# Kernel tuning notes

Measured on AMD Instinct MI355X. Metric: run time of the kernel, lower is better.

The kernel has to match this reference:

```python
import jax, jax.numpy as jnp
import numpy as np

B, T_ENC, FEAT, H, W2V, T_DEC, V = 32, 80, 4096, 256, 256, 30, 32000


def lstm_cell(x, h, c, w_ih, w_hh, b_ih, b_hh):
    # PyTorch LSTMCell: gates order i, f, g, o
    g = x @ w_ih.T + h @ w_hh.T + b_ih + b_hh
    i, f, gg, o = jnp.split(g, 4, axis=-1)
    c_new = jax.nn.sigmoid(f) * c + jax.nn.sigmoid(i) * jnp.tanh(gg)
    h_new = jax.nn.sigmoid(o) * jnp.tanh(c_new)
    return h_new, c_new


def setup_inputs() -> dict:
    key = jax.random.key(0)
    ks = jax.random.split(key, 13)
    s = 0.05
    return {
        'feat': jax.random.normal(ks[0], (B, T_ENC, FEAT), jnp.float32),
        'caption': jax.random.normal(ks[1], (B, T_DEC, W2V), jnp.float32),
        'caption_one_hot': jax.random.normal(ks[2], (B, T_DEC, V), jnp.float32),
        'keep_rate': 1,
        'w_ih1': jax.random.normal(ks[3], (4 * H, FEAT), jnp.float32) * s,
        'w_hh1': jax.random.normal(ks[4], (4 * H, H), jnp.float32) * s,
        'b_ih1': jax.random.normal(ks[5], (4 * H,), jnp.float32) * s,
        'b_hh1': jax.random.normal(ks[6], (4 * H,), jnp.float32) * s,
        'w_ih2': jax.random.normal(ks[7], (4 * H, H + W2V), jnp.float32) * s,
        'w_hh2': jax.random.normal(ks[8], (4 * H, H), jnp.float32) * s,
        'b_ih2': jax.random.normal(ks[9], (4 * H,), jnp.float32) * s,
        'b_hh2': jax.random.normal(ks[10], (4 * H,), jnp.float32) * s,
        'w_out': jax.random.normal(ks[11], (V, H), jnp.float32) * s,
        'b_out': jax.random.normal(ks[12], (V,), jnp.float32) * s,
    }


def reference(feat, caption, caption_one_hot, keep_rate,
              w_ih1, w_hh1, b_ih1, b_hh1,
              w_ih2, w_hh2, b_ih2, b_hh2,
              w_out, b_out):
    zeros_h = jnp.zeros((B, H), feat.dtype)
    pad1 = jnp.zeros((B, FEAT), feat.dtype)

    # ---------------- encoder: 80 steps ----------------
    def enc_step(carry, x_t):
        h1, c1, h2, c2 = carry
        h1, c1 = lstm_cell(x_t, h1, c1, w_ih1, w_hh1, b_ih1, b_hh1)
        h2, c2 = lstm_cell(jnp.concatenate([zeros_h, h1], axis=1), h2, c2,
                           w_ih2, w_hh2, b_ih2, b_hh2)
        return (h1, c1, h2, c2), h2

    (h1, c1, h2, c2), enc_h2 = jax.lax.scan(
        enc_step, (zeros_h, zeros_h, zeros_h, zeros_h),
        jnp.transpose(feat, (1, 0, 2)))
    enc_h2 = jnp.transpose(enc_h2, (1, 0, 2))  # [B, 80, H]

    # ---------------- decoder: teacher forcing (coin>=100 never fires) ----
    targets = jnp.argmax(caption_one_hot, axis=-1)  # [B, T_DEC]

    def dec_step(carry, xs):
        h1, c1, h2, c2, loss = carry
        word_t, tgt_t = xs  # [B, W2V], [B]
        h1, c1 = lstm_cell(pad1, h1, c1, w_ih1, w_hh1, b_ih1, b_hh1)
        h2n, c2 = lstm_cell(jnp.concatenate([word_t, h1], axis=1), h2, c2,
                            w_ih2, w_hh2, b_ih2, b_hh2)
        logits = h2n @ w_out.T + b_out  # [B, V]
        logp = jax.nn.log_softmax(logits, axis=-1)
        ce = -jnp.take_along_axis(logp, tgt_t[:, None], axis=1)[:, 0]
        loss = loss + jnp.mean(ce) / B  # sum(mean-CE)/batch, per original
        # attention: scores of encoder h2 states against current h2
        attn = jax.nn.softmax(jnp.einsum('bsh,bh->bs', enc_h2, h2n), axis=-1)
        ctx = jnp.einsum('bs,bsh->bh', attn, enc_h2)  # replaces h2 for next step
        return (h1, c1, ctx, c2, loss), None

    xs = (jnp.transpose(caption[:, :T_DEC - 1, :], (1, 0, 2)),
          jnp.transpose(targets[:, 1:T_DEC], (1, 0)))
    (h1, c1, h2, c2, total_loss), _ = jax.lax.scan(
        dec_step, (h1, c1, h2, c2, jnp.float32(0.0)), xs)
    return total_loss
```

## Files before the change

### kernel.cpp

```cpp
#include <hip/hip_runtime.h>
#include <hip/hip_bf16.h>
#include <math.h>

#define BB 32
#define TE 80
#define FEAT 4096
#define HH 256
#define W2V 256
#define TD 30
#define VV 32000
#define G4 1024

typedef unsigned short u16;
typedef unsigned int u32;
using f32x4 = __attribute__((ext_vector_type(4))) float;
using bf16x8 = __attribute__((ext_vector_type(8))) short;
using f16x2 = __attribute__((ext_vector_type(2))) _Float16;

#define SENT 0xFFFFFFFFu
#define NANF 0x7FC00000u

__device__ __forceinline__ float sigm(float x) { return 1.0f / (1.0f + expf(-x)); }
__device__ __forceinline__ u16 f2bf(float f) {
  u32 u = __float_as_uint(f);
  u32 r = (u + 0x7FFFu + ((u >> 16) & 1u)) >> 16;
  return (u16)r;
}
__device__ __forceinline__ u32 packh2(float lo, float hi) {
  f16x2 v = {(_Float16)lo, (_Float16)hi};
  return __builtin_bit_cast(u32, v);
}

#define AT_LOAD(p)     __hip_atomic_load((p), __ATOMIC_RELAXED, __HIP_MEMORY_SCOPE_AGENT)
#define AT_STORE(p, v) __hip_atomic_store((p), (v), __ATOMIC_RELAXED, __HIP_MEMORY_SCOPE_AGENT)

__device__ __forceinline__ float fdot2h(f16x2 a, f16x2 b, float c) {
#if __has_builtin(__builtin_amdgcn_fdot2)
  return __builtin_amdgcn_fdot2(a, b, c, false);
#else
  return c + (float)a[0] * (float)b[0] + (float)a[1] * (float)b[1];
#endif
}

__global__ __launch_bounds__(256) void prep_kernel(
    const float* __restrict__ feat, const float* __restrict__ w_ih1,
    const float* __restrict__ w_ih2, const float* __restrict__ caption,
    const float* __restrict__ onehot,
    const float* __restrict__ b_ih1, const float* __restrict__ b_hh1,
    const float* __restrict__ b_ih2, const float* __restrict__ b_hh2,
    u16* __restrict__ featb, u16* __restrict__ w_ih1b,
    u16* __restrict__ w_ih2lb, u16* __restrict__ capb,
    float* __restrict__ bias1, float* __restrict__ bias2,
    u32* __restrict__ H1H, u32* __restrict__ H2H, u32* __restrict__ A2P,
    float* __restrict__ loss, int* __restrict__ ctrs,
    int* __restrict__ targets) {
  int blk = blockIdx.x, tid = threadIdx.x;
  if (blk < 928) {
    int k = blk;
    int s = (k >> 5) + 1, b = k & 31;
    const float* row = &onehot[((size_t)b * TD + s) * VV];
    float bv = -INFINITY;
    int bi = 0x7fffffff;
    for (int v = tid; v < VV; v += 256) {
      float x = row[v];
      if (x > bv || (x == bv && v < bi)) { bv = x; bi = v; }
    }
    __shared__ float sv[256];
    __shared__ int si[256];
    sv[tid] = bv; si[tid] = bi;
    __syncthreads();
    for (int off = 128; off; off >>= 1) {
      if (tid < off) {
        float ov = sv[tid + off]; int oi = si[tid + off];
        if (ov > sv[tid] || (ov == sv[tid] && oi < si[tid])) { sv[tid] = ov; si[tid] = oi; }
      }
      __syncthreads();
    }
    if (tid == 0) targets[k] = si[0];
  } else if (blk < 3488) {
    int i0 = (blk - 928) * 1024 + tid;
#pragma unroll
    for (int ii = 0; ii < 4; ++ii) {
      int i = i0 + ii * 256;
      float4 v = *(const float4*)&feat[(size_t)i * 4];
      *(ushort4*)&featb[(size_t)i * 4] =
          make_ushort4(f2bf(v.x), f2bf(v.y), f2bf(v.z), f2bf(v.w));
    }
  } else if (blk < 4512) {
    int i0 = (blk - 3488) * 1024 + tid;
#pragma unroll
    for (int ii = 0; ii < 4; ++ii) {
      int i = i0 + ii * 256;
      float4 v = *(const float4*)&w_ih1[(size_t)i * 4];
      *(ushort4*)&w_ih1b[(size_t)i * 4] =
          make_ushort4(f2bf(v.x), f2bf(v.y), f2bf(v.z), f2bf(v.w));
    }
  } else if (blk < 4576) {
    int i0 = (blk - 4512) * 1024 + tid;
#pragma unroll
    for (int ii = 0; ii < 4; ++ii) {
      int i = i0 + ii * 256;
      int row = i >> 6, c = (i & 63) * 4;
      float4 v = *(const float4*)&w_ih2[(size_t)row * 512 + c];
      *(ushort4*)&w_ih2lb[(size_t)row * 256 + c] =
          make_ushort4(f2bf(v.x), f2bf(v.y), f2bf(v.z), f2bf(v.w));
    }
  } else if (blk < 4636) {
    int i0 = (blk - 4576) * 1024 + tid;
#pragma unroll
    for (int ii = 0; ii < 4; ++ii) {
      int i = i0 + ii * 256;
      float4 v = *(const float4*)&caption[(size_t)i * 4];
      *(ushort4*)&capb[(size_t)i * 4] =
          make_ushort4(f2bf(v.x), f2bf(v.y), f2bf(v.z), f2bf(v.w));
    }
  } else if (blk < 5076) {
    int i = (blk - 4636) * 256 + tid;
    uint4 z = {0u, 0u, 0u, 0u};
    uint4 s = {SENT, SENT, SENT, SENT};
    uint4 v = (i < 1024) ? z : s;
    ((uint4*)H1H)[i] = v;
    ((uint4*)H2H)[i] = v;
  } else if (blk < 5956) {
    int i0 = (blk - 5076) * 1024 + tid;
    uint4 s = {NANF, NANF, NANF, NANF};
#pragma unroll
    for (int ii = 0; ii < 4; ++ii) ((uint4*)A2P)[i0 + ii * 256] = s;
  } else {
    for (int i = tid; i < 1024; i += 256) {
      bias1[i] = b_ih1[i] + b_hh1[i];
      bias2[i] = b_ih2[i] + b_hh2[i];
    }
    if (tid == 0) { *loss = 0.0f; ctrs[0] = 0; ctrs[32] = 0; }
  }
}

#define GBM 128
#define GBN 128
#define GBK 64
#define LDSTR 72

__device__ void gemm_x1_body(char* smem, int bx, int by,
                             const u16* __restrict__ Ab, const u16* __restrict__ Bw,
                             const float* __restrict__ bias, float* __restrict__ C) {
  u16* As = (u16*)smem;
  u16* Bs = (u16*)(smem + 18432);
  int tid = threadIdx.x;
  int rBase = by * GBM;
  int nBase = bx * GBN;
  int lane = tid & 63, w = tid >> 6;
  int wrow = (w >> 1) * 64, wcol = (w & 1) * 64;
  int lrow = lane & 15, lk = (lane >> 4) * 8;

  f32x4 acc[4][4];
#pragma unroll
  for (int m = 0; m < 4; ++m)
#pragma unroll
    for (int n = 0; n < 4; ++n) acc[m][n] = (f32x4){0.f, 0.f, 0.f, 0.f};

  for (int k0 = 0; k0 < FEAT; k0 += GBK) {
#pragma unroll
    for (int i = 0; i < 4; ++i) {
      int f = i * 256 + tid;
      int r = f >> 3, c8 = f & 7;
      *(uint4*)&As[r * LDSTR + c8 * 8] =
          *(const uint4*)&Ab[(size_t)(rBase + r) * FEAT + k0 + c8 * 8];
    }
#pragma unroll
    for (int i = 0; i < 4; ++i) {
      int f = i * 256 + tid;
      int r = f >> 3, c8 = f & 7;
      *(uint4*)&Bs[r * LDSTR + c8 * 8] =
          *(const uint4*)&Bw[(size_t)(nBase + r) * FEAT + k0 + c8 * 8];
    }
    __syncthreads();
#pragma unroll
    for (int s2 = 0; s2 < 2; ++s2) {
      bf16x8 af[4], bfr[4];
#pragma unroll
      for (int m = 0; m < 4; ++m)
        af[m] = *(const bf16x8*)&As[(wrow + m * 16 + lrow) * LDSTR + s2 * 32 + lk];
#pragma unroll
      for (int n = 0; n < 4; ++n)
        bfr[n] = *(const bf16x8*)&Bs[(wcol + n * 16 + lrow) * LDSTR + s2 * 32 + lk];
#pragma unroll
      for (int m = 0; m < 4; ++m)
#pragma unroll
        for (int n = 0; n < 4; ++n)
          acc[m][n] = __builtin_amdgcn_mfma_f32_16x16x32_bf16(
              af[m], bfr[n], acc[m][n], 0, 0, 0);
    }
    __syncthreads();
  }
  int orow = (lane >> 4) * 4;
  int ocol = lane & 15;
#pragma unroll
  for (int m = 0; m < 4; ++m)
#pragma unroll
    for (int n = 0; n < 4; ++n) {
      int cidx = nBase + wcol + n * 16 + ocol;
      float bv = bias[cidx];
#pragma unroll
      for (int q = 0; q < 4; ++q) {
        int r = rBase + wrow + m * 16 + orow + q;
        C[(size_t)r * G4 + cidx] = acc[m][n][q] + bv;
      }
    }
}

__device__ void xw2_body(char* smem, int nb, int t,
                         const u16* __restrict__ capb, const u16* __restrict__ w_ih2lb,
                         const float* __restrict__ bias2, float* __restrict__ XW2) {
  u16* As = (u16*)smem;
  u16* Bs = (u16*)(smem + 16896);
  int tid = threadIdx.x;
  int nBase = nb * 64;
#pragma unroll
  for (int it = 0; it < 4; ++it) {
    int i = it * 256 + tid;
    int r = i >> 5, c8 = i & 31;
    *(uint4*)&As[r * 264 + c8 * 8] =
        *(const uint4*)&capb[((size_t)r * TD + t) * 256 + c8 * 8];
  }
#pragma unroll
  for (int it = 0; it < 8; ++it) {
    int i = it * 256 + tid;
    int r = i >> 5, c8 = i & 31;
    *(uint4*)&Bs[r * 264 + c8 * 8] =
        *(const uint4*)&w_ih2lb[(size_t)(nBase + r) * 256 + c8 * 8];
  }
  __syncthreads();
  int lane = tid & 63, w = tid >> 6;
  int lrow = lane & 15, lk = (lane >> 4) * 8;
  f32x4 acc[2];
  acc[0] = (f32x4){0.f, 0.f, 0.f, 0.f};
  acc[1] = (f32x4){0.f, 0.f, 0.f, 0.f};
#pragma unroll
  for (int ks = 0; ks < 8; ++ks) {
    bf16x8 bfr = *(const bf16x8*)&Bs[(w * 16 + lrow) * 264 + ks * 32 + lk];
#pragma unroll
    for (int m = 0; m < 2; ++m) {
      bf16x8 af = *(const bf16x8*)&As[(m * 16 + lrow) * 264 + ks * 32 + lk];
      acc[m] = __builtin_amdgcn_mfma_f32_16x16x32_bf16(af, bfr, acc[m], 0, 0, 0);
    }
  }
  int col = nBase + w * 16 + (lane & 15);
  float bv = bias2[col];
  int orow = (lane >> 4) * 4;
#pragma unroll
  for (int m = 0; m < 2; ++m)
#pragma unroll
    for (int q = 0; q < 4; ++q) {
      int bb = m * 16 + orow + q;
      XW2[((size_t)t * 32 + bb) * G4 + col] = acc[m][q] + bv;
    }
}

__global__ __launch_bounds__(256) void gemms_kernel(
    const u16* __restrict__ featb, const u16* __restrict__ w_ih1b,
    const float* __restrict__ bias1, float* __restrict__ X1,
    const u16* __restrict__ capb, const u16* __restrict__ w_ih2lb,
    const float* __restrict__ bias2, float* __restrict__ XW2) {
  __shared__ __align__(16) char smem[50688];
  int blk = blockIdx.x;
  if (blk < 160) {
    gemm_x1_body(smem, blk & 7, blk >> 3, featb, w_ih1b, bias1, X1);
  } else {
    int k = blk - 160;
    xw2_body(smem, k & 15, k >> 4, capb, w_ih2lb, bias2, XW2);
  }
}

struct RP {
  const float *X1, *XW2, *bias1, *bias2;
  const float *w_hh1, *w_ih2, *w_hh2;
  u32* H1H;
  u32* H2H;
  u32* A2P;
  u16* H2NB;
};

__global__ __launch_bounds__(512, 1) void recurrent_kernel(RP p) {
  __shared__ float encL[TE][257];
  __shared__ __align__(16) f16x2 hS[128];
  __shared__ float tmp2[256];
  __shared__ float gb[256];
  __shared__ float a2pS[256];
  __shared__ float hnew[64];
  __shared__ float sc[80];
  __shared__ float red[4];
  int bid = blockIdx.x, tid = threadIdx.x;
  bool isL1 = bid < 128;
  int lb = isL1 ? bid : bid - 128;
  int b = lb >> 2, q = lb & 3;
  int r2 = tid >> 1, half = tid & 1;
  int g = r2 >> 6, jj = r2 & 63;
  int grow = (g << 8) + (q << 6) + jj;
  int jf = (q << 6) + tid;

  if (isL1) {
    f16x2 wA[64], wB[64];
    {
      const float4* sA = (const float4*)(p.w_hh1 + (size_t)grow * 256 + half * 128);
      const float4* sB = (const float4*)(p.w_ih2 + (size_t)grow * 512 + 256 + half * 128);
#pragma unroll
      for (int k = 0; k < 32; ++k) {
        float4 v = sA[k];
        wA[k * 2 + 0] = f16x2{(_Float16)v.x, (_Float16)v.y};
        wA[k * 2 + 1] = f16x2{(_Float16)v.z, (_Float16)v.w};
        float4 u = sB[k];
        wB[k * 2 + 0] = f16x2{(_Float16)u.x, (_Float16)u.y};
        wB[k * 2 + 1] = f16x2{(_Float16)u.z, (_Float16)u.w};
      }
    }
    float c1 = 0.f;
    float b1v0 = 0, b1v1 = 0, b1v2 = 0, b1v3 = 0;
    if (tid < 64) {
      b1v0 = p.bias1[jf]; b1v1 = p.bias1[256 + jf];
      b1v2 = p.bias1[512 + jf]; b1v3 = p.bias1[768 + jf];
    }
    for (int T = 0; T <= 109; ++T) {
      float x0 = b1v0, x1 = b1v1, x2 = b1v2, x3 = b1v3;
      if (tid < 64 && T < TE) {
        const float* xb = &p.X1[((size_t)b * TE + T) * G4 + jf];
        x0 = xb[0]; x1 = xb[256]; x2 = xb[512]; x3 = xb[768];
      }
      if (tid < 128) {
        const u32* src = &p.H1H[((size_t)T * 32 + b) * 128 + tid];
        u32 v = AT_LOAD(src);
        int gd = 0;
        while (v == SENT && ++gd < (1 << 24)) {
          __builtin_amdgcn_s_sleep(1);
          v = AT_LOAD(src);
        }
        hS[tid] = __builtin_bit_cast(f16x2, v);
      }
      __syncthreads();
      float a1 = 0.f, a2 = 0.f;
      {
        const uint4* hv = ((const uint4*)hS) + half * 16;
#pragma unroll
        for (int k = 0; k < 16; ++k) {
          uint4 uu = hv[k];
          f16x2 e0 = __builtin_bit_cast(f16x2, uu.x), e1 = __builtin_bit_cast(f16x2, uu.y);
          f16x2 e2 = __builtin_bit_cast(f16x2, uu.z), e3 = __builtin_bit_cast(f16x2, uu.w);
          a1 = fdot2h(e0, wA[k * 4 + 0], a1);
          a2 = fdot2h(e0, wB[k * 4 + 0], a2);
          a1 = fdot2h(e1, wA[k * 4 + 1], a1);
          a2 = fdot2h(e1, wB[k * 4 + 1], a2);
          a1 = fdot2h(e2, wA[k * 4 + 2], a1);
          a2 = fdot2h(e2, wB[k * 4 + 2], a2);
          a1 = fdot2h(e3, wA[k * 4 + 3], a1);
          a2 = fdot2h(e3, wB[k * 4 + 3], a2);
        }
      }
      a1 += __shfl_xor(a1, 1);
      a2 += __shfl_xor(a2, 1);
      if (half == 0) {
        gb[r2] = a1;
        if (T >= 1)
          AT_STORE(&p.A2P[((size_t)T * 32 + b) * 1024 + grow], __float_as_uint(a2));
      }
      __syncthreads();
      if (T <= 108) {
        if (tid < 64) {
          float gi = gb[tid] + x0;
          float gf = gb[64 + tid] + x1;
          float gG = gb[128 + tid] + x2;
          float go = gb[192 + tid] + x3;
          c1 = sigm(gf) * c1 + sigm(gi) * tanhf(gG);
          hnew[tid] = sigm(go) * tanhf(c1);
        }
        if (tid < 32) {
          u32 pk = packh2(hnew[2 * tid], hnew[2 * tid + 1]);
          AT_STORE(&p.H1H[((size_t)(T + 1) * 32 + b) * 128 + (q << 5) + tid], pk);
        }
      }
    }
  } else {
    f16x2 wC[64];
    {
      const float4* sC = (const float4*)(p.w_hh2 + (size_t)grow * 256 + half * 128);
#pragma unroll
      for (int k = 0; k < 32; ++k) {
        float4 u = sC[k];
        wC[k * 2 + 0] = f16x2{(_Float16)u.x, (_Float16)u.y};
        wC[k * 2 + 1] = f16x2{(_Float16)u.z, (_Float16)u.w};
      }
    }
    float c2 = 0.f;
    float b2v0 = 0, b2v1 = 0, b2v2 = 0, b2v3 = 0;
    if (tid < 64) {
      b2v0 = p.bias2[jf]; b2v1 = p.bias2[256 + jf];
      b2v2 = p.bias2[512 + jf]; b2v3 = p.bias2[768 + jf];
    }
    for (int U = 1; U <= 109; ++U) {
      float x0 = b2v0, x1 = b2v1, x2 = b2v2, x3 = b2v3;
      if (tid < 64 && U >= 81) {
        const float* xb = &p.XW2[((size_t)(U - 81) * 32 + b) * G4 + jf];
        x0 = xb[0]; x1 = xb[256]; x2 = xb[512]; x3 = xb[768];
      }
      if (tid < 128) {
        const u32* src = &p.H2H[((size_t)(U - 1) * 32 + b) * 128 + tid];
        u32 v = AT_LOAD(src);
        int gd = 0;
        while (v == SENT && ++gd < (1 << 26)) v = AT_LOAD(src);
        f16x2 hp = __builtin_bit_cast(f16x2, v);
        hS[tid] = hp;
        tmp2[2 * tid] = (float)hp[0];
        tmp2[2 * tid + 1] = (float)hp[1];
      } else if (tid < 384) {
        int rr = tid - 128;
        int growp = ((rr >> 6) << 8) + (q << 6) + (rr & 63);
        const u32* src = &p.A2P[((size_t)U * 32 + b) * 1024 + growp];
        u32 v = AT_LOAD(src);
        int gd = 0;
        while (v == NANF && ++gd < (1 << 24)) {
          __builtin_amdgcn_s_sleep(1);
          v = AT_LOAD(src);
        }
        a2pS[rr] = __uint_as_float(v);
      }
      __syncthreads();
      float a2p0 = 0, a2p1 = 0, a2p2 = 0, a2p3 = 0;
      if (tid < 64) {
        a2p0 = a2pS[tid]; a2p1 = a2pS[64 + tid];
        a2p2 = a2pS[128 + tid]; a2p3 = a2pS[192 + tid];
      }
      if (U <= 81) {
        if (U >= 2 && tid < 256) encL[U - 2][tid] = tmp2[tid];
      } else {
        float a = 0.f;
        if (tid < TE) {
          const float* e = &encL[tid][0];
#pragma unroll 8
          for (int k2 = 0; k2 < 256; ++k2) a += e[k2] * tmp2[k2];
        }
        float av = (tid < TE) ? a : -INFINITY;
#pragma unroll
        for (int d = 32; d; d >>= 1) av = fmaxf(av, __shfl_xor(av, d));
        if (tid == 0) red[0] = av;
        if (tid == 64) red[1] = av;
        __syncthreads();
        float m = fmaxf(red[0], red[1]);
        float e2 = (tid < TE) ? expf(a - m) : 0.f;
        float sv = e2;
#pragma unroll
        for (int d = 32; d; d >>= 1) sv += __shfl_xor(sv, d);
        if (tid == 0) red[2] = sv;
        if (tid == 64) red[3] = sv;
        __syncthreads();
        float inv = 1.0f / (red[2] + red[3]);
        if (tid < TE) sc[tid] = e2 * inv;
        __syncthreads();
        if (tid < 256) {
          float acc = 0.f;
          for (int t2 = 0; t2 < TE; ++t2) acc += sc[t2] * encL[t2][tid];
          tmp2[tid] = acc;
        }
        __syncthreads();
        if (tid < 128)
          hS[tid] = f16x2{(_Float16)tmp2[2 * tid], (_Float16)tmp2[2 * tid + 1]};
        __syncthreads();
      }
      float a2 = 0.f;
      {
        const uint4* hv = ((const uint4*)hS) + half * 16;
#pragma unroll
        for (int k = 0; k < 16; ++k) {
          uint4 uu = hv[k];
          a2 = fdot2h(__builtin_bit_cast(f16x2, uu.x), wC[k * 4 + 0], a2);
          a2 = fdot2h(__builtin_bit_cast(f16x2, uu.y), wC[k * 4 + 1], a2);
          a2 = fdot2h(__builtin_bit_cast(f16x2, uu.z), wC[k * 4 + 2], a2);
          a2 = fdot2h(__builtin_bit_cast(f16x2, uu.w), wC[k * 4 + 3], a2);
        }
      }
      a2 += __shfl_xor(a2, 1);
      if (half == 0) gb[r2] = a2;
      __syncthreads();
      if (tid < 64) {
        float gi = gb[tid] + a2p0 + x0;
        float gf = gb[64 + tid] + a2p1 + x1;
        float gG = gb[128 + tid] + a2p2 + x2;
        float go = gb[192 + tid] + a2p3 + x3;
        c2 = sigm(gf) * c2 + sigm(gi) * tanhf(gG);
        float h = sigm(go) * tanhf(c2);
        hnew[tid] = h;
        if (U >= 81)
          p.H2NB[((size_t)(U - 81) * 32 + b) * 256 + jf] = f2bf(h);
      }
      if (tid < 32) {
        u32 pk = packh2(hnew[2 * tid], hnew[2 * tid + 1]);
        AT_STORE(&p.H2H[((size_t)U * 32 + b) * 128 + (q << 5) + tid], pk);
      }
    }
  }
}

__global__ __launch_bounds__(256, 1) void logits_final_kernel(
    const u16* __restrict__ H2NB, const float* __restrict__ w_out,
    const float* __restrict__ b_out, const int* __restrict__ targets,
    u32* __restrict__ pmaxA, u32* __restrict__ psumA, u32* __restrict__ tgtv,
    float* __restrict__ loss, int* __restrict__ ctrs, float* __restrict__ out) {
  __shared__ __align__(16) u16 bS[32768];
  __shared__ __align__(16) u16 aS[32 * 264];
  __shared__ int tS[32];
  __shared__ float sm[256];
  int tid = threadIdx.x, bid = blockIdx.x;
#pragma unroll
  for (int it = 0; it < 16; ++it) {
    int id = it * 256 + tid;
    int nt = id >> 9, rr = (id >> 5) & 15, kg = id & 31;
    int n = bid * 128 + nt * 16 + rr;
    const float* src = &w_out[(size_t)n * 256 + kg * 8];
    float4 v0 = *(const float4*)src;
    float4 v1 = *(const float4*)(src + 4);
    u16* dst = &bS[(size_t)((nt * 32 + kg) * 16 + rr) * 8];
    *(ushort4*)dst = make_ushort4(f2bf(v0.x), f2bf(v0.y), f2bf(v0.z), f2bf(v0.w));
    *(ushort4*)(dst + 4) = make_ushort4(f2bf(v1.x), f2bf(v1.y), f2bf(v1.z), f2bf(v1.w));
  }
  int wid = tid >> 6, lane = tid & 63, lcol = lane & 15, lk = lane >> 4;
  float bo[2];
#pragma unroll
  for (int n = 0; n < 2; ++n) bo[n] = b_out[(bid * 8 + wid * 2 + n) * 16 + lcol];

  for (int rg = 0; rg < 29; ++rg) {
    __syncthreads();
    for (int i = tid; i < 1024; i += 256) {
      int r = i >> 5, c8 = i & 31;
      *(uint4*)&aS[r * 264 + c8 * 8] =
          *(const uint4*)&H2NB[(size_t)rg * 8192 + r * 256 + c8 * 8];
    }
    if (tid < 32) tS[tid] = targets[rg * 32 + tid];
    __syncthreads();
    f32x4 acc[2][2];
#pragma unroll
    for (int m = 0; m < 2; ++m)
#pragma unroll
      for (int n = 0; n < 2; ++n) acc[m][n] = (f32x4){0.f, 0.f, 0.f, 0.f};
#pragma unroll
    for (int ks = 0; ks < 8; ++ks) {
      bf16x8 a0 = *(const bf16x8*)&aS[lcol * 264 + ks * 32 + lk * 8];
      bf16x8 a1 = *(const bf16x8*)&aS[(16 + lcol) * 264 + ks * 32 + lk * 8];
      bf16x8 b0 = *(const bf16x8*)&bS[(wid * 2) * 4096 + ((ks * 4 + lk) * 16 + lcol) * 8];
      bf16x8 b1 = *(const bf16x8*)&bS[(wid * 2 + 1) * 4096 + ((ks * 4 + lk) * 16 + lcol) * 8];
      acc[0][0] = __builtin_amdgcn_mfma_f32_16x16x32_bf16(a0, b0, acc[0][0], 0, 0, 0);
      acc[0][1] = __builtin_amdgcn_mfma_f32_16x16x32_bf16(a0, b1, acc[0][1], 0, 0, 0);
      acc[1][0] = __builtin_amdgcn_mfma_f32_16x16x32_bf16(a1, b0, acc[1][0], 0, 0, 0);
      acc[1][1] = __builtin_amdgcn_mfma_f32_16x16x32_bf16(a1, b1, acc[1][1], 0, 0, 0);
    }
    int nbase = (bid * 8 + wid * 2) * 16 + lcol;
#pragma unroll
    for (int m = 0; m < 2; ++m) {
      float pm[4], psv[4];
#pragma unroll
      for (int qq = 0; qq < 4; ++qq) {
        float v0 = acc[m][0][qq] + bo[0];
        float v1 = acc[m][1][qq] + bo[1];
        int r = m * 16 + lk * 4 + qq;
        int tg = tS[r];
        if (tg == nbase) AT_STORE(&tgtv[rg * 32 + r], __float_as_uint(v0));
        if (tg == nbase + 16) AT_STORE(&tgtv[rg * 32 + r], __float_as_uint(v1));
        float mx = fmaxf(v0, v1);
#pragma unroll
        for (int d = 1; d < 16; d <<= 1) mx = fmaxf(mx, __shfl_xor(mx, d));
        float e = expf(v0 - mx) + expf(v1 - mx);
#pragma unroll
        for (int d = 1; d < 16; d <<= 1) e += __shfl_xor(e, d);
        pm[qq] = mx;
        psv[qq] = e;
      }
      if (lcol == 0) {
        int chunk = bid * 4 + wid;
#pragma unroll
        for (int qq = 0; qq < 4; ++qq) {
          int r2 = rg * 32 + m * 16 + lk * 4 + qq;
          AT_STORE(&pmaxA[(size_t)r2 * 1000 + chunk], __float_as_uint(pm[qq]));
          AT_STORE(&psumA[(size_t)r2 * 1000 + chunk], __float_as_uint(psv[qq]));
        }
      }
    }
  }
  asm volatile("s_waitcnt vmcnt(0)" ::: "memory");
  __syncthreads();
  if (tid == 0) {
    __hip_atomic_fetch_add(&ctrs[0], 1, __ATOMIC_RELEASE, __HIP_MEMORY_SCOPE_AGENT);
    int gd = 0;
    while (__hip_atomic_load(&ctrs[0], __ATOMIC_ACQUIRE, __HIP_MEMORY_SCOPE_AGENT) < 250 &&
           ++gd < (1 << 26))
      __builtin_amdgcn_s_sleep(2);
  }
  __syncthreads();
#pragma unroll
  for (int k = 0; k < 4; ++k) {
    int row = bid * 4 + k;
    if (row < 928) {
      const u32* pm = pmaxA + (size_t)row * 1000;
      const u32* psv = psumA + (size_t)row * 1000;
      float m = -INFINITY;
      for (int c = tid; c < 1000; c += 256) m = fmaxf(m, __uint_as_float(AT_LOAD(&pm[c])));
      sm[tid] = m;
      __syncthreads();
      for (int off = 128; off; off >>= 1) {
        if (tid < off) sm[tid] = fmaxf(sm[tid], sm[tid + off]);
        __syncthreads();
      }
      float M = sm[0];
      __syncthreads();
      float s = 0.f;
      for (int c = tid; c < 1000; c += 256)
        s += __uint_as_float(AT_LOAD(&psv[c])) * expf(__uint_as_float(AT_LOAD(&pm[c])) - M);
      sm[tid] = s;
      __syncthreads();
      for (int off = 128; off; off >>= 1) {
        if (tid < off) sm[tid] += sm[tid + off];
        __syncthreads();
      }
      if (tid == 0) {
        float tv = __uint_as_float(AT_LOAD(&tgtv[row]));
        atomicAdd(loss, (M + logf(sm[0]) - tv) * (1.0f / 1024.0f));
      }
      __syncthreads();
    }
  }
  asm volatile("s_waitcnt vmcnt(0)" ::: "memory");
  if (tid == 0) {
    int old = __hip_atomic_fetch_add(&ctrs[32], 1, __ATOMIC_ACQ_REL, __HIP_MEMORY_SCOPE_AGENT);
    if (old == 249) out[0] = __uint_as_float(AT_LOAD((u32*)loss));
  }
}

extern "C" void kernel_launch(void* const* d_in, const int* in_sizes, int n_in,
                              void* d_out, int out_size, void* d_ws, size_t ws_size,
                              hipStream_t stream) {
  (void)in_sizes; (void)n_in; (void)out_size; (void)ws_size;
  const float* feat    = (const float*)d_in[0];
  const float* caption = (const float*)d_in[1];
  const float* onehot  = (const float*)d_in[2];
  const float* w_ih1   = (const float*)d_in[4];
  const float* w_hh1   = (const float*)d_in[5];
  const float* b_ih1   = (const float*)d_in[6];
  const float* b_hh1   = (const float*)d_in[7];
  const float* w_ih2   = (const float*)d_in[8];
  const float* w_hh2   = (const float*)d_in[9];
  const float* b_ih2   = (const float*)d_in[10];
  const float* b_hh2   = (const float*)d_in[11];
  const float* w_out   = (const float*)d_in[12];
  const float* b_out   = (const float*)d_in[13];

  char* p = (char*)d_ws;
  auto alloc = [&](size_t bytes) {
    char* r = p;
    p += (bytes + 255) & ~(size_t)255;
    return r;
  };
  float* X1      = (float*)alloc(2560ull * 1024 * 4);
  float* XW2     = (float*)alloc(29ull * 32 * 1024 * 4);
  float* bias1   = (float*)alloc(1024 * 4);
  float* bias2   = (float*)alloc(1024 * 4);
  u32*   H1H     = (u32*)alloc(110ull * 32 * 128 * 4);
  u32*   H2H     = (u32*)alloc(110ull * 32 * 128 * 4);
  u32*   A2P     = (u32*)alloc(110ull * 32 * 1024 * 4);
  u16*   H2NB    = (u16*)alloc(29ull * 8192 * 2);
  u32*   pmaxA   = (u32*)alloc(928ull * 1000 * 4);
  u32*   psumA   = (u32*)alloc(928ull * 1000 * 4);
  u32*   tgtv    = (u32*)alloc(928 * 4);
  float* lossacc = (float*)alloc(256);
  int*   ctrs    = (int*)alloc(256);
  int*   targets = (int*)alloc(29 * 32 * 4);
  u16*   featb   = (u16*)alloc(2560ull * 4096 * 2);
  u16*   w_ih1b  = (u16*)alloc(1024ull * 4096 * 2);
  u16*   w_ih2lb = (u16*)alloc(1024ull * 256 * 2);
  u16*   capb    = (u16*)alloc(32ull * 30 * 256 * 2);

  prep_kernel<<<5957, 256, 0, stream>>>(
      feat, w_ih1, w_ih2, caption, onehot,
      b_ih1, b_hh1, b_ih2, b_hh2,
      featb, w_ih1b, w_ih2lb, capb,
      bias1, bias2, H1H, H2H, A2P, lossacc, ctrs, targets);
  gemms_kernel<<<624, 256, 0, stream>>>(featb, w_ih1b, bias1, X1,
                                        capb, w_ih2lb, bias2, XW2);

  RP rp;
  rp.X1 = X1; rp.XW2 = XW2; rp.bias1 = bias1; rp.bias2 = bias2;
  rp.w_hh1 = w_hh1; rp.w_ih2 = w_ih2; rp.w_hh2 = w_hh2;
  rp.H1H = H1H; rp.H2H = H2H; rp.A2P = A2P; rp.H2NB = H2NB;
  void* args[] = {&rp};
  hipLaunchCooperativeKernel((const void*)recurrent_kernel, dim3(256), dim3(512),
                             args, 0, stream);

  logits_final_kernel<<<250, 256, 0, stream>>>(H2NB, w_out, b_out, targets,
                                               pmaxA, psumA, tgtv, lossacc, ctrs,
                                               (float*)d_out);
}
```

Measured before the change: 687.5 us.

## Fuse input GEMMs into prep and recurrent kernels; precompute attention gate projections

New measurement: 704.1 us. 2.4% more time.

```diff
diff --git a/kernel.cpp b/kernel.cpp
--- a/kernel.cpp
+++ b/kernel.cpp
@@ -49,11 +49,12 @@
     const float* __restrict__ b_ih1, const float* __restrict__ b_hh1,
     const float* __restrict__ b_ih2, const float* __restrict__ b_hh2,
     u16* __restrict__ featb, u16* __restrict__ w_ih1b,
-    u16* __restrict__ w_ih2lb, u16* __restrict__ capb,
+    float* __restrict__ XW2,
     float* __restrict__ bias1, float* __restrict__ bias2,
     u32* __restrict__ H1H, u32* __restrict__ H2H, u32* __restrict__ A2P,
     float* __restrict__ loss, int* __restrict__ ctrs,
     int* __restrict__ targets) {
+  __shared__ __align__(16) char psm[50688];
   int blk = blockIdx.x, tid = threadIdx.x;
   if (blk < 928) {
     int k = blk;
@@ -65,8 +66,8 @@
       float x = row[v];
       if (x > bv || (x == bv && v < bi)) { bv = x; bi = v; }
     }
-    __shared__ float sv[256];
-    __shared__ int si[256];
+    float* sv = (float*)psm;
+    int* si = (int*)(psm + 1024);
     sv[tid] = bv; si[tid] = bi;
     __syncthreads();
     for (int off = 128; off; off >>= 1) {
@@ -95,34 +96,67 @@
       *(ushort4*)&w_ih1b[(size_t)i * 4] =
           make_ushort4(f2bf(v.x), f2bf(v.y), f2bf(v.z), f2bf(v.w));
     }
-  } else if (blk < 4576) {
-    int i0 = (blk - 4512) * 1024 + tid;
-#pragma unroll
-    for (int ii = 0; ii < 4; ++ii) {
-      int i = i0 + ii * 256;
-      int row = i >> 6, c = (i & 63) * 4;
-      float4 v = *(const float4*)&w_ih2[(size_t)row * 512 + c];
-      *(ushort4*)&w_ih2lb[(size_t)row * 256 + c] =
-          make_ushort4(f2bf(v.x), f2bf(v.y), f2bf(v.z), f2bf(v.w));
-    }
-  } else if (blk < 4636) {
-    int i0 = (blk - 4576) * 1024 + tid;
-#pragma unroll
-    for (int ii = 0; ii < 4; ++ii) {
-      int i = i0 + ii * 256;
-      float4 v = *(const float4*)&caption[(size_t)i * 4];
-      *(ushort4*)&capb[(size_t)i * 4] =
-          make_ushort4(f2bf(v.x), f2bf(v.y), f2bf(v.z), f2bf(v.w));
-    }
-  } else if (blk < 5076) {
-    int i = (blk - 4636) * 256 + tid;
+  } else if (blk < 4976) {
+    int k = blk - 4512, nb = k & 15, t = k >> 4;
+    u16* As = (u16*)psm;
+    u16* Bs = (u16*)(psm + 16896);
+    int nBase = nb * 64;
+#pragma unroll
+    for (int it = 0; it < 4; ++it) {
+      int i = it * 256 + tid;
+      int r = i >> 5, c8 = i & 31;
+      const float* src = &caption[((size_t)r * TD + t) * 256 + c8 * 8];
+      float4 v0 = *(const float4*)src;
+      float4 v1 = *(const float4*)(src + 4);
+      u16* dst = &As[r * 264 + c8 * 8];
+      *(ushort4*)dst = make_ushort4(f2bf(v0.x), f2bf(v0.y), f2bf(v0.z), f2bf(v0.w));
+      *(ushort4*)(dst + 4) = make_ushort4(f2bf(v1.x), f2bf(v1.y), f2bf(v1.z), f2bf(v1.w));
+    }
+#pragma unroll
+    for (int it = 0; it < 8; ++it) {
+      int i = it * 256 + tid;
+      int r = i >> 5, c8 = i & 31;
+      const float* src = &w_ih2[(size_t)(nBase + r) * 512 + c8 * 8];
+      float4 v0 = *(const float4*)src;
+      float4 v1 = *(const float4*)(src + 4);
+      u16* dst = &Bs[r * 264 + c8 * 8];
+      *(ushort4*)dst = make_ushort4(f2bf(v0.x), f2bf(v0.y), f2bf(v0.z), f2bf(v0.w));
+      *(ushort4*)(dst + 4) = make_ushort4(f2bf(v1.x), f2bf(v1.y), f2bf(v1.z), f2bf(v1.w));
+    }
+    __syncthreads();
+    int lane = tid & 63, w = tid >> 6;
+    int lrow = lane & 15, lk = (lane >> 4) * 8;
+    f32x4 acc[2];
+    acc[0] = (f32x4){0.f, 0.f, 0.f, 0.f};
+    acc[1] = (f32x4){0.f, 0.f, 0.f, 0.f};
+#pragma unroll
+    for (int ks = 0; ks < 8; ++ks) {
+      bf16x8 bfr = *(const bf16x8*)&Bs[(w * 16 + lrow) * 264 + ks * 32 + lk];
+#pragma unroll
+      for (int m = 0; m < 2; ++m) {
+        bf16x8 af = *(const bf16x8*)&As[(m * 16 + lrow) * 264 + ks * 32 + lk];
+        acc[m] = __builtin_amdgcn_mfma_f32_16x16x32_bf16(af, bfr, acc[m], 0, 0, 0);
+      }
+    }
+    int col = nBase + w * 16 + (lane & 15);
+    float bv = b_ih2[col] + b_hh2[col];
+    int orow = (lane >> 4) * 4;
+#pragma unroll
+    for (int m = 0; m < 2; ++m)
+#pragma unroll
+      for (int qq = 0; qq < 4; ++qq) {
+        int bb = m * 16 + orow + qq;
+        XW2[((size_t)t * 32 + bb) * G4 + col] = acc[m][qq] + bv;
+      }
+  } else if (blk < 5416) {
+    int i = (blk - 4976) * 256 + tid;
     uint4 z = {0u, 0u, 0u, 0u};
     uint4 s = {SENT, SENT, SENT, SENT};
     uint4 v = (i < 1024) ? z : s;
     ((uint4*)H1H)[i] = v;
     ((uint4*)H2H)[i] = v;
-  } else if (blk < 5956) {
-    int i0 = (blk - 5076) * 1024 + tid;
+  } else if (blk < 6296) {
+    int i0 = (blk - 5416) * 1024 + tid;
     uint4 s = {NANF, NANF, NANF, NANF};
 #pragma unroll
     for (int ii = 0; ii < 4; ++ii) ((uint4*)A2P)[i0 + ii * 256] = s;
@@ -135,144 +169,9 @@
   }
 }
 
-#define GBM 128
-#define GBN 128
-#define GBK 64
-#define LDSTR 72
-
-__device__ void gemm_x1_body(char* smem, int bx, int by,
-                             const u16* __restrict__ Ab, const u16* __restrict__ Bw,
-                             const float* __restrict__ bias, float* __restrict__ C) {
-  u16* As = (u16*)smem;
-  u16* Bs = (u16*)(smem + 18432);
-  int tid = threadIdx.x;
-  int rBase = by * GBM;
-  int nBase = bx * GBN;
-  int lane = tid & 63, w = tid >> 6;
-  int wrow = (w >> 1) * 64, wcol = (w & 1) * 64;
-  int lrow = lane & 15, lk = (lane >> 4) * 8;
-
-  f32x4 acc[4][4];
-#pragma unroll
-  for (int m = 0; m < 4; ++m)
-#pragma unroll
-    for (int n = 0; n < 4; ++n) acc[m][n] = (f32x4){0.f, 0.f, 0.f, 0.f};
-
-  for (int k0 = 0; k0 < FEAT; k0 += GBK) {
-#pragma unroll
-    for (int i = 0; i < 4; ++i) {
-      int f = i * 256 + tid;
-      int r = f >> 3, c8 = f & 7;
-      *(uint4*)&As[r * LDSTR + c8 * 8] =
-          *(const uint4*)&Ab[(size_t)(rBase + r) * FEAT + k0 + c8 * 8];
-    }
-#pragma unroll
-    for (int i = 0; i < 4; ++i) {
-      int f = i * 256 + tid;
-      int r = f >> 3, c8 = f & 7;
-      *(uint4*)&Bs[r * LDSTR + c8 * 8] =
-          *(const uint4*)&Bw[(size_t)(nBase + r) * FEAT + k0 + c8 * 8];
-    }
-    __syncthreads();
-#pragma unroll
-    for (int s2 = 0; s2 < 2; ++s2) {
-      bf16x8 af[4], bfr[4];
-#pragma unroll
-      for (int m = 0; m < 4; ++m)
-        af[m] = *(const bf16x8*)&As[(wrow + m * 16 + lrow) * LDSTR + s2 * 32 + lk];
-#pragma unroll
-      for (int n = 0; n < 4; ++n)
-        bfr[n] = *(const bf16x8*)&Bs[(wcol + n * 16 + lrow) * LDSTR + s2 * 32 + lk];
-#pragma unroll
-      for (int m = 0; m < 4; ++m)
-#pragma unroll
-        for (int n = 0; n < 4; ++n)
-          acc[m][n] = __builtin_amdgcn_mfma_f32_16x16x32_bf16(
-              af[m], bfr[n], acc[m][n], 0, 0, 0);
-    }
-    __syncthreads();
-  }
-  int orow = (lane >> 4) * 4;
-  int ocol = lane & 15;
-#pragma unroll
-  for (int m = 0; m < 4; ++m)
-#pragma unroll
-    for (int n = 0; n < 4; ++n) {
-      int cidx = nBase + wcol + n * 16 + ocol;
-      float bv = bias[cidx];
-#pragma unroll
-      for (int q = 0; q < 4; ++q) {
-        int r = rBase + wrow + m * 16 + orow + q;
-        C[(size_t)r * G4 + cidx] = acc[m][n][q] + bv;
-      }
-    }
-}
-
-__device__ void xw2_body(char* smem, int nb, int t,
-                         const u16* __restrict__ capb, const u16* __restrict__ w_ih2lb,
-                         const float* __restrict__ bias2, float* __restrict__ XW2) {
-  u16* As = (u16*)smem;
-  u16* Bs = (u16*)(smem + 16896);
-  int tid = threadIdx.x;
-  int nBase = nb * 64;
-#pragma unroll
-  for (int it = 0; it < 4; ++it) {
-    int i = it * 256 + tid;
-    int r = i >> 5, c8 = i & 31;
-    *(uint4*)&As[r * 264 + c8 * 8] =
-        *(const uint4*)&capb[((size_t)r * TD + t) * 256 + c8 * 8];
-  }
-#pragma unroll
-  for (int it = 0; it < 8; ++it) {
-    int i = it * 256 + tid;
-    int r = i >> 5, c8 = i & 31;
-    *(uint4*)&Bs[r * 264 + c8 * 8] =
-        *(const uint4*)&w_ih2lb[(size_t)(nBase + r) * 256 + c8 * 8];
-  }
-  __syncthreads();
-  int lane = tid & 63, w = tid >> 6;
-  int lrow = lane & 15, lk = (lane >> 4) * 8;
-  f32x4 acc[2];
-  acc[0] = (f32x4){0.f, 0.f, 0.f, 0.f};
-  acc[1] = (f32x4){0.f, 0.f, 0.f, 0.f};
-#pragma unroll
-  for (int ks = 0; ks < 8; ++ks) {
-    bf16x8 bfr = *(const bf16x8*)&Bs[(w * 16 + lrow) * 264 + ks * 32 + lk];
-#pragma unroll
-    for (int m = 0; m < 2; ++m) {
-      bf16x8 af = *(const bf16x8*)&As[(m * 16 + lrow) * 264 + ks * 32 + lk];
-      acc[m] = __builtin_amdgcn_mfma_f32_16x16x32_bf16(af, bfr, acc[m], 0, 0, 0);
-    }
-  }
-  int col = nBase + w * 16 + (lane & 15);
-  float bv = bias2[col];
-  int orow = (lane >> 4) * 4;
-#pragma unroll
-  for (int m = 0; m < 2; ++m)
-#pragma unroll
-    for (int q = 0; q < 4; ++q) {
-      int bb = m * 16 + orow + q;
-      XW2[((size_t)t * 32 + bb) * G4 + col] = acc[m][q] + bv;
-    }
-}
-
-__global__ __launch_bounds__(256) void gemms_kernel(
-    const u16* __restrict__ featb, const u16* __restrict__ w_ih1b,
-    const float* __restrict__ bias1, float* __restrict__ X1,
-    const u16* __restrict__ capb, const u16* __restrict__ w_ih2lb,
-    const float* __restrict__ bias2, float* __restrict__ XW2) {
-  __shared__ __align__(16) char smem[50688];
-  int blk = blockIdx.x;
-  if (blk < 160) {
-    gemm_x1_body(smem, blk & 7, blk >> 3, featb, w_ih1b, bias1, X1);
-  } else {
-    int k = blk - 160;
-    xw2_body(smem, k & 15, k >> 4, capb, w_ih2lb, bias2, XW2);
-  }
-}
-
 struct RP {
-  const float *X1, *XW2, *bias1, *bias2;
+  const float *XW2, *bias1, *bias2;
+  const u16 *featb, *w_ih1b;
   const float *w_hh1, *w_ih2, *w_hh2;
   u32* H1H;
   u32* H2H;
@@ -281,14 +180,7 @@
 };
 
 __global__ __launch_bounds__(512, 1) void recurrent_kernel(RP p) {
-  __shared__ float encL[TE][257];
-  __shared__ __align__(16) f16x2 hS[128];
-  __shared__ float tmp2[256];
-  __shared__ float gb[256];
-  __shared__ float a2pS[256];
-  __shared__ float hnew[64];
-  __shared__ float sc[80];
-  __shared__ float red[4];
+  __shared__ __align__(16) char smem[133120];
   int bid = blockIdx.x, tid = threadIdx.x;
   bool isL1 = bid < 128;
   int lb = isL1 ? bid : bid - 128;
@@ -296,9 +188,67 @@
   int r2 = tid >> 1, half = tid & 1;
   int g = r2 >> 6, jj = r2 & 63;
   int grow = (g << 8) + (q << 6) + jj;
-  int jf = (q << 6) + tid;
 
   if (isL1) {
+    u16* As = (u16*)smem;
+    u16* Bs = (u16*)(smem + 11520);
+    float* X1L = (float*)(smem + 48384);
+    f16x2* hS = (f16x2*)(smem + 130624);
+    float* gb = (float*)(smem + 131136);
+    float* hnew = (float*)(smem + 132160);
+    {
+      int lane = tid & 63, w = tid >> 6;
+      int lrow = lane & 15, lk = (lane >> 4) * 8;
+      f32x4 acc[5][2];
+#pragma unroll
+      for (int m = 0; m < 5; ++m)
+#pragma unroll
+        for (int n = 0; n < 2; ++n) acc[m][n] = (f32x4){0.f, 0.f, 0.f, 0.f};
+      for (int k0 = 0; k0 < FEAT; k0 += 64) {
+        for (int f = tid; f < 640; f += 512) {
+          int r = f >> 3, c8 = f & 7;
+          *(uint4*)&As[r * 72 + c8 * 8] =
+              *(const uint4*)&p.featb[((size_t)(b * 80 + r)) * FEAT + k0 + c8 * 8];
+        }
+#pragma unroll
+        for (int it = 0; it < 4; ++it) {
+          int f = it * 512 + tid;
+          int r = f >> 3, c8 = f & 7;
+          int gg = r >> 6, u = r & 63;
+          *(uint4*)&Bs[r * 72 + c8 * 8] =
+              *(const uint4*)&p.w_ih1b[((size_t)(gg * 256 + q * 64 + u)) * FEAT + k0 + c8 * 8];
+        }
+        __syncthreads();
+#pragma unroll
+        for (int ks = 0; ks < 2; ++ks) {
+          bf16x8 bfr[2];
+#pragma unroll
+          for (int n = 0; n < 2; ++n)
+            bfr[n] = *(const bf16x8*)&Bs[((w * 2 + n) * 16 + lrow) * 72 + ks * 32 + lk];
+#pragma unroll
+          for (int m = 0; m < 5; ++m) {
+            bf16x8 af = *(const bf16x8*)&As[(m * 16 + lrow) * 72 + ks * 32 + lk];
+#pragma unroll
+            for (int n = 0; n < 2; ++n)
+              acc[m][n] = __builtin_amdgcn_mfma_f32_16x16x32_bf16(af, bfr[n], acc[m][n], 0, 0, 0);
+          }
+        }
+        __syncthreads();
+      }
+      int lcol = lane & 15, orow = (lane >> 4) * 4;
+#pragma unroll
+      for (int m = 0; m < 5; ++m)
+#pragma unroll
+        for (int n = 0; n < 2; ++n) {
+          int cn = (w * 2 + n) * 16 + lcol;
+          int gc = (cn >> 6) * 256 + q * 64 + (cn & 63);
+          float bv = p.bias1[gc];
+#pragma unroll
+          for (int qq = 0; qq < 4; ++qq)
+            X1L[(m * 16 + orow + qq) * 257 + cn] = acc[m][n][qq] + bv;
+        }
+      __syncthreads();
+    }
     f16x2 wA[64], wB[64];
     {
       const float4* sA = (const float4*)(p.w_hh1 + (size_t)grow * 256 + half * 128);
@@ -316,14 +266,18 @@
     float c1 = 0.f;
     float b1v0 = 0, b1v1 = 0, b1v2 = 0, b1v3 = 0;
     if (tid < 64) {
-      b1v0 = p.bias1[jf]; b1v1 = p.bias1[256 + jf];
-      b1v2 = p.bias1[512 + jf]; b1v3 = p.bias1[768 + jf];
+      b1v0 = p.bias1[(q << 6) + tid];
+      b1v1 = p.bias1[256 + (q << 6) + tid];
+      b1v2 = p.bias1[512 + (q << 6) + tid];
+      b1v3 = p.bias1[768 + (q << 6) + tid];
     }
     for (int T = 0; T <= 109; ++T) {
       float x0 = b1v0, x1 = b1v1, x2 = b1v2, x3 = b1v3;
       if (tid < 64 && T < TE) {
-        const float* xb = &p.X1[((size_t)b * TE + T) * G4 + jf];
-        x0 = xb[0]; x1 = xb[256]; x2 = xb[512]; x3 = xb[768];
+        x0 = X1L[T * 257 + tid];
+        x1 = X1L[T * 257 + 64 + tid];
+        x2 = X1L[T * 257 + 128 + tid];
+        x3 = X1L[T * 257 + 192 + tid];
       }
       if (tid < 128) {
         const u32* src = &p.H1H[((size_t)T * 32 + b) * 128 + tid];
@@ -378,6 +332,15 @@
       }
     }
   } else {
+    f16x2* encLh = (f16x2*)smem;
+    u16* g2Lh = (u16*)(smem + 42240);
+    f16x2* hS = (f16x2*)(smem + 84480);
+    float* a2pS = (float*)(smem + 85536);
+    float* gb = (float*)(smem + 86560);
+    float* hnew = (float*)(smem + 87584);
+    float* ps = (float*)(smem + 87840);
+    float* sc = (float*)(smem + 89120);
+    float* red = (float*)(smem + 89440);
     f16x2 wC[64];
     {
       const float4* sC = (const float4*)(p.w_hh2 + (size_t)grow * 256 + half * 128);
@@ -391,13 +354,15 @@
     float c2 = 0.f;
     float b2v0 = 0, b2v1 = 0, b2v2 = 0, b2v3 = 0;
     if (tid < 64) {
-      b2v0 = p.bias2[jf]; b2v1 = p.bias2[256 + jf];
-      b2v2 = p.bias2[512 + jf]; b2v3 = p.bias2[768 + jf];
+      b2v0 = p.bias2[(q << 6) + tid];
+      b2v1 = p.bias2[256 + (q << 6) + tid];
+      b2v2 = p.bias2[512 + (q << 6) + tid];
+      b2v3 = p.bias2[768 + (q << 6) + tid];
     }
     for (int U = 1; U <= 109; ++U) {
       float x0 = b2v0, x1 = b2v1, x2 = b2v2, x3 = b2v3;
       if (tid < 64 && U >= 81) {
-        const float* xb = &p.XW2[((size_t)(U - 81) * 32 + b) * G4 + jf];
+        const float* xb = &p.XW2[((size_t)(U - 81) * 32 + b) * G4 + (q << 6) + tid];
         x0 = xb[0]; x1 = xb[256]; x2 = xb[512]; x3 = xb[768];
       }
       if (tid < 128) {
@@ -407,8 +372,7 @@
         while (v == SENT && ++gd < (1 << 26)) v = AT_LOAD(src);
         f16x2 hp = __builtin_bit_cast(f16x2, v);
         hS[tid] = hp;
-        tmp2[2 * tid] = (float)hp[0];
-        tmp2[2 * tid + 1] = (float)hp[1];
+        if (U >= 2 && U <= 81) encLh[(U - 2) * 132 + tid] = hp;
       } else if (tid < 384) {
         int rr = tid - 128;
         int growp = ((rr >> 6) << 8) + (q << 6) + (rr & 63);
@@ -428,43 +392,7 @@
         a2p2 = a2pS[128 + tid]; a2p3 = a2pS[192 + tid];
       }
       if (U <= 81) {
-        if (U >= 2 && tid < 256) encL[U - 2][tid] = tmp2[tid];
-      } else {
-        float a = 0.f;
-        if (tid < TE) {
-          const float* e = &encL[tid][0];
-#pragma unroll 8
-          for (int k2 = 0; k2 < 256; ++k2) a += e[k2] * tmp2[k2];
-        }
-        float av = (tid < TE) ? a : -INFINITY;
-#pragma unroll
-        for (int d = 32; d; d >>= 1) av = fmaxf(av, __shfl_xor(av, d));
-        if (tid == 0) red[0] = av;
-        if (tid == 64) red[1] = av;
-        __syncthreads();
-        float m = fmaxf(red[0], red[1]);
-        float e2 = (tid < TE) ? expf(a - m) : 0.f;
-        float sv = e2;
-#pragma unroll
-        for (int d = 32; d; d >>= 1) sv += __shfl_xor(sv, d);
-        if (tid == 0) red[2] = sv;
-        if (tid == 64) red[3] = sv;
-        __syncthreads();
-        float inv = 1.0f / (red[2] + red[3]);
-        if (tid < TE) sc[tid] = e2 * inv;
-        __syncthreads();
-        if (tid < 256) {
-          float acc = 0.f;
-          for (int t2 = 0; t2 < TE; ++t2) acc += sc[t2] * encL[t2][tid];
-          tmp2[tid] = acc;
-        }
-        __syncthreads();
-        if (tid < 128)
-          hS[tid] = f16x2{(_Float16)tmp2[2 * tid], (_Float16)tmp2[2 * tid + 1]};
-        __syncthreads();
-      }
-      float a2 = 0.f;
-      {
+        float a2 = 0.f;
         const uint4* hv = ((const uint4*)hS) + half * 16;
 #pragma unroll
         for (int k = 0; k < 16; ++k) {
@@ -474,10 +402,53 @@
           a2 = fdot2h(__builtin_bit_cast(f16x2, uu.z), wC[k * 4 + 2], a2);
           a2 = fdot2h(__builtin_bit_cast(f16x2, uu.w), wC[k * 4 + 3], a2);
         }
-      }
-      a2 += __shfl_xor(a2, 1);
-      if (half == 0) gb[r2] = a2;
-      __syncthreads();
+        a2 += __shfl_xor(a2, 1);
+        if (half == 0) {
+          gb[r2] = a2;
+          if (U >= 2) g2Lh[(U - 2) * 264 + r2] = __builtin_bit_cast(u16, (_Float16)a2);
+        }
+        __syncthreads();
+      } else {
+        if (tid < 320) {
+          int t = tid >> 2, kq = tid & 3;
+          float a = 0.f;
+          const f16x2* e = &encLh[t * 132];
+#pragma unroll
+          for (int i = 0; i < 32; ++i)
+            a = fdot2h(e[kq + 4 * i], hS[kq + 4 * i], a);
+          ps[tid] = a;
+        }
+        __syncthreads();
+        float sco = 0.f;
+        if (tid < TE) sco = ps[4 * tid] + ps[4 * tid + 1] + ps[4 * tid + 2] + ps[4 * tid + 3];
+        float av = (tid < TE) ? sco : -INFINITY;
+#pragma unroll
+        for (int d = 32; d; d >>= 1) av = fmaxf(av, __shfl_xor(av, d));
+        if (tid == 0) red[0] = av;
+        if (tid == 64) red[1] = av;
+        __syncthreads();
+        float m = fmaxf(red[0], red[1]);
+        float e2 = (tid < TE) ? expf(sco - m) : 0.f;
+        float sv = e2;
+#pragma unroll
+        for (int d = 32; d; d >>= 1) sv += __shfl_xor(sv, d);
+        if (tid == 0) red[2] = sv;
+        if (tid == 64) red[3] = sv;
+        __syncthreads();
+        float inv = 1.0f / (red[2] + red[3]);
+        if (tid < TE) sc[tid] = e2 * inv;
+        __syncthreads();
+        float acc = 0.f;
+#pragma unroll 8
+        for (int k = 0; k < 40; ++k) {
+          int t = 2 * k + half;
+          float g2v = (float)__builtin_bit_cast(_Float16, g2Lh[t * 264 + r2]);
+          acc = fmaf(sc[t], g2v, acc);
+        }
+        acc += __shfl_xor(acc, 1);
+        if (half == 0) gb[r2] = acc;
+        __syncthreads();
+      }
       if (tid < 64) {
         float gi = gb[tid] + a2p0 + x0;
         float gf = gb[64 + tid] + a2p1 + x1;
@@ -487,7 +458,7 @@
         float h = sigm(go) * tanhf(c2);
         hnew[tid] = h;
         if (U >= 81)
-          p.H2NB[((size_t)(U - 81) * 32 + b) * 256 + jf] = f2bf(h);
+          p.H2NB[((size_t)(U - 81) * 32 + b) * 256 + (q << 6) + tid] = f2bf(h);
       }
       if (tid < 32) {
         u32 pk = packh2(hnew[2 * tid], hnew[2 * tid + 1]);
@@ -654,7 +625,6 @@
     p += (bytes + 255) & ~(size_t)255;
     return r;
   };
-  float* X1      = (float*)alloc(2560ull * 1024 * 4);
   float* XW2     = (float*)alloc(29ull * 32 * 1024 * 4);
   float* bias1   = (float*)alloc(1024 * 4);
   float* bias2   = (float*)alloc(1024 * 4);
@@ -670,19 +640,16 @@
   int*   targets = (int*)alloc(29 * 32 * 4);
   u16*   featb   = (u16*)alloc(2560ull * 4096 * 2);
   u16*   w_ih1b  = (u16*)alloc(1024ull * 4096 * 2);
-  u16*   w_ih2lb = (u16*)alloc(1024ull * 256 * 2);
-  u16*   capb    = (u16*)alloc(32ull * 30 * 256 * 2);
-
-  prep_kernel<<<5957, 256, 0, stream>>>(
+
+  prep_kernel<<<6297, 256, 0, stream>>>(
       feat, w_ih1, w_ih2, caption, onehot,
       b_ih1, b_hh1, b_ih2, b_hh2,
-      featb, w_ih1b, w_ih2lb, capb,
+      featb, w_ih1b, XW2,
       bias1, bias2, H1H, H2H, A2P, lossacc, ctrs, targets);
-  gemms_kernel<<<624, 256, 0, stream>>>(featb, w_ih1b, bias1, X1,
-                                        capb, w_ih2lb, bias2, XW2);
 
   RP rp;
-  rp.X1 = X1; rp.XW2 = XW2; rp.bias1 = bias1; rp.bias2 = bias2;
+  rp.XW2 = XW2; rp.bias1 = bias1; rp.bias2 = bias2;
+  rp.featb = featb; rp.w_ih1b = w_ih1b;
   rp.w_hh1 = w_hh1; rp.w_ih2 = w_ih2; rp.w_hh2 = w_hh2;
   rp.H1H = H1H; rp.H2H = H2H; rp.A2P = A2P; rp.H2NB = H2NB;
   void* args[] = {&rp};
```
